# Kernel optimization log

Hardware: AMD Instinct MI355X
Metric: run time of the kernel (lower is better)

The kernel has to match this reference:

```python
import jax, jax.numpy as jnp
import numpy as np
from jax import lax

HEADS = 4
DIM_HEAD = 32
IH = IW = 64
IH_RED = 32  # image_size // reduce_ratio; F.interpolate(size=int) -> square output


def dw_conv(t, w):
    # depthwise 3x3, stride 1, padding 1, NCHW; w: [C,1,3,3]
    return lax.conv_general_dilated(t, w, (1, 1), [(1, 1), (1, 1)],
                                    feature_group_count=t.shape[1],
                                    dimension_numbers=("NCHW", "OIHW", "NCHW"))


def pw_conv(t, w):
    # pointwise 1x1 conv as einsum; w: [O,C,1,1]
    return jnp.einsum("oc,bchw->bohw", w[:, :, 0, 0], t)


def resize_bilinear_ac(t, out_h, out_w):
    # bilinear, align_corners=True, t: [B,C,H,W]
    H, W = t.shape[-2], t.shape[-1]
    ys = jnp.linspace(0.0, H - 1.0, out_h)
    xs = jnp.linspace(0.0, W - 1.0, out_w)
    y0 = jnp.floor(ys).astype(jnp.int32)
    x0 = jnp.floor(xs).astype(jnp.int32)
    y1 = jnp.minimum(y0 + 1, H - 1)
    x1 = jnp.minimum(x0 + 1, W - 1)
    wy = (ys - y0).astype(t.dtype)[None, None, :, None]
    wx = (xs - x0).astype(t.dtype)[None, None, None, :]
    row = t[:, :, y0, :] * (1 - wy) + t[:, :, y1, :] * wy  # [B,C,OH,W]
    out = row[:, :, :, x0] * (1 - wx) + row[:, :, :, x1] * wx  # [B,C,OH,OW]
    return out


def to_heads(t):
    # [B, h*d, H, W] -> [B, h, H*W, d]
    B, _, H, W = t.shape
    return t.reshape(B, HEADS, DIM_HEAD, H * W).transpose(0, 1, 3, 2)


def setup_inputs() -> dict:
    key = jax.random.key(0)
    ks = jax.random.split(key, 7)
    inner = HEADS * DIM_HEAD  # 128
    return {
        "x": jax.random.normal(ks[0], (8, 256, 16, 16), jnp.float32),
        "skip": jax.random.normal(ks[1], (8, 128, 64, 64), jnp.float32),
        "dw_q": jax.random.normal(ks[2], (128, 1, 3, 3), jnp.float32) * 0.1,
        "pw_q": jax.random.normal(ks[3], (inner, 128, 1, 1), jnp.float32) * 0.05,
        "dw_kv": jax.random.normal(ks[4], (256, 1, 3, 3), jnp.float32) * 0.1,
        "pw_kv": jax.random.normal(ks[5], (2 * inner, 256, 1, 1), jnp.float32) * 0.05,
        "w_out": jax.random.normal(ks[6], (128, inner, 1, 1), jnp.float32) * 0.05,
    }


def reference(x, skip, dw_q, pw_q, dw_kv, pw_kv, w_out):
    scale = DIM_HEAD ** -0.5
    q = to_heads(pw_conv(dw_conv(skip, dw_q), pw_q))  # [B,h,4096,d]
    kv = pw_conv(dw_conv(x, dw_kv), pw_kv)            # [B,2*inner,16,16]
    k, v = jnp.split(kv, 2, axis=1)
    k = to_heads(resize_bilinear_ac(k, IH_RED, IH_RED))  # [B,h,1024,d]
    v = to_heads(resize_bilinear_ac(v, IH_RED, IH_RED))
    dots = jnp.einsum("bhqd,bhkd->bhqk", q, k) * scale
    attn = jax.nn.softmax(dots, axis=-1)
    out = jnp.einsum("bhqk,bhkd->bhqd", attn, v)  # [B,h,4096,d]
    B = out.shape[0]
    out = out.transpose(0, 1, 3, 2).reshape(B, HEADS * DIM_HEAD, IH, IW)
    return pw_conv(out, w_out)
```

## Files before the change

kernel.cpp:

```cpp
#include <hip/hip_runtime.h>
#include <hip/hip_bf16.h>

typedef __attribute__((ext_vector_type(4))) float f32x4;
typedef __attribute__((ext_vector_type(8))) short bf16x8;
typedef __attribute__((ext_vector_type(4))) short s16x4;

#define DEV static __device__ __forceinline__

DEV int imin(int a, int b) { return a < b ? a : b; }

DEV short f2bf(float f) {
  union { float f; unsigned u; } v; v.f = f;
  unsigned r = (v.u + 0x7fffu + ((v.u >> 16) & 1u)) >> 16;
  return (short)r;
}

DEV bf16x8 cvt8(const float* __restrict__ p) {
  f32x4 a = *reinterpret_cast<const f32x4*>(p);
  f32x4 b = *reinterpret_cast<const f32x4*>(p + 4);
  bf16x8 r;
  r[0] = f2bf(a[0]); r[1] = f2bf(a[1]); r[2] = f2bf(a[2]); r[3] = f2bf(a[3]);
  r[4] = f2bf(b[0]); r[5] = f2bf(b[1]); r[6] = f2bf(b[2]); r[7] = f2bf(b[3]);
  return r;
}

__global__ __launch_bounds__(256) void k_qgen(const float* __restrict__ skip,
    const float* __restrict__ dw_q, const float* __restrict__ pw_q,
    short* __restrict__ Q) {
  const int b = blockIdx.y;
  const int y = blockIdx.x;
  __shared__ __align__(16) short dwT[64][136];
  const int t = threadIdx.x;
  {
    const int x = t & 63;
    const int cg = t >> 6;
    for (int i = 0; i < 32; ++i) {
      const int c = cg * 32 + i;
      const float* sp = skip + (b * 128 + c) * 4096;
      const float* wp = dw_q + c * 9;
      float acc = 0.f;
      #pragma unroll
      for (int ky = 0; ky < 3; ++ky) {
        const int yy = y + ky - 1;
        if (yy < 0 || yy > 63) continue;
        #pragma unroll
        for (int kx = 0; kx < 3; ++kx) {
          const int xx = x + kx - 1;
          if (xx < 0 || xx > 63) continue;
          acc += sp[yy * 64 + xx] * wp[ky * 3 + kx];
        }
      }
      dwT[x][c] = f2bf(acc);
    }
  }
  __syncthreads();
  const int w = t >> 6, l = t & 63, lr = l & 15, lg = l >> 4;
  f32x4 acc[4][2];
  #pragma unroll
  for (int pt = 0; pt < 4; ++pt)
    #pragma unroll
    for (int ot = 0; ot < 2; ++ot) acc[pt][ot] = f32x4{0.f, 0.f, 0.f, 0.f};
  #pragma unroll
  for (int kk = 0; kk < 4; ++kk) {
    const int c0 = kk * 32 + lg * 8;
    bf16x8 bfr[2];
    #pragma unroll
    for (int ot = 0; ot < 2; ++ot) {
      const int o = (2 * w + ot) * 16 + lr;
      bfr[ot] = cvt8(pw_q + o * 128 + c0);
    }
    #pragma unroll
    for (int pt = 0; pt < 4; ++pt) {
      bf16x8 afr = *reinterpret_cast<const bf16x8*>(&dwT[pt * 16 + lr][c0]);
      #pragma unroll
      for (int ot = 0; ot < 2; ++ot)
        acc[pt][ot] = __builtin_amdgcn_mfma_f32_16x16x32_bf16(afr, bfr[ot], acc[pt][ot], 0, 0, 0);
    }
  }
  const float sc = 0.17677669529663689f;
  #pragma unroll
  for (int pt = 0; pt < 4; ++pt)
    #pragma unroll
    for (int ot = 0; ot < 2; ++ot)
      #pragma unroll
      for (int r = 0; r < 4; ++r) {
        const int pix = y * 64 + pt * 16 + lg * 4 + r;
        const int o = (2 * w + ot) * 16 + lr;
        Q[(b * 4096 + pix) * 128 + o] = f2bf(acc[pt][ot][r] * sc);
      }
}

__global__ __launch_bounds__(256) void k_kvgen(const float* __restrict__ x,
    const float* __restrict__ dw_kv, const float* __restrict__ pw_kv,
    float* __restrict__ kv16) {
  const int b = blockIdx.y;
  const int pq = blockIdx.x;
  __shared__ __align__(16) short dwxT[16][264];
  const int t = threadIdx.x;
  {
    const int pl = t & 15;
    const int cg = t >> 4;
    const int py = pq, px = pl;
    for (int i = 0; i < 16; ++i) {
      const int c = cg * 16 + i;
      const float* sp = x + (b * 256 + c) * 256;
      const float* wp = dw_kv + c * 9;
      float acc = 0.f;
      #pragma unroll
      for (int ky = 0; ky < 3; ++ky) {
        const int yy = py + ky - 1;
        if (yy < 0 || yy > 15) continue;
        #pragma unroll
        for (int kx = 0; kx < 3; ++kx) {
          const int xx = px + kx - 1;
          if (xx < 0 || xx > 15) continue;
          acc += sp[yy * 16 + xx] * wp[ky * 3 + kx];
        }
      }
      dwxT[pl][c] = f2bf(acc);
    }
  }
  __syncthreads();
  const int w = t >> 6, l = t & 63, lr = l & 15, lg = l >> 4;
  f32x4 acc[4];
  #pragma unroll
  for (int ot = 0; ot < 4; ++ot) acc[ot] = f32x4{0.f, 0.f, 0.f, 0.f};
  #pragma unroll
  for (int kk = 0; kk < 8; ++kk) {
    const int c0 = kk * 32 + lg * 8;
    bf16x8 bfr = *reinterpret_cast<const bf16x8*>(&dwxT[lr][c0]);
    #pragma unroll
    for (int ot = 0; ot < 4; ++ot) {
      const int o = (w * 4 + ot) * 16 + lr;
      bf16x8 afr = cvt8(pw_kv + o * 256 + c0);
      acc[ot] = __builtin_amdgcn_mfma_f32_16x16x32_bf16(afr, bfr, acc[ot], 0, 0, 0);
    }
  }
  #pragma unroll
  for (int ot = 0; ot < 4; ++ot)
    #pragma unroll
    for (int r = 0; r < 4; ++r) {
      const int o = (w * 4 + ot) * 16 + lg * 4 + r;
      const int pix = pq * 16 + lr;
      kv16[(b * 256 + o) * 256 + pix] = acc[ot][r];
    }
}

DEV float bilin16(const float* __restrict__ p, int key) {
  const int oy = key >> 5, ox = key & 31;
  const float s = 15.f / 31.f;
  const float syf = oy * s, sxf = ox * s;
  const int y0 = (int)syf, x0 = (int)sxf;
  const int y1 = imin(y0 + 1, 15), x1 = imin(x0 + 1, 15);
  const float wy = syf - (float)y0, wx = sxf - (float)x0;
  const float r0 = p[y0 * 16 + x0] * (1.f - wx) + p[y0 * 16 + x1] * wx;
  const float r1 = p[y1 * 16 + x0] * (1.f - wx) + p[y1 * 16 + x1] * wx;
  return r0 * (1.f - wy) + r1 * wy;
}

__global__ __launch_bounds__(256) void k_resize(const float* __restrict__ kv16,
    short* __restrict__ K, short* __restrict__ Vt) {
  const int idx = blockIdx.x * 256 + threadIdx.x;
  {
    const int d = idx & 31;
    int rest = idx >> 5;
    const int key = rest & 1023; rest >>= 10;
    const int h = rest & 3; const int b = rest >> 2;
    const int ch = h * 32 + d;
    K[idx] = f2bf(bilin16(kv16 + (b * 256 + ch) * 256, key));
  }
  {
    const int key = idx & 1023;
    int rest = idx >> 10;
    const int d = rest & 31; rest >>= 5;
    const int h = rest & 3; const int b = rest >> 2;
    const int ch = 128 + h * 32 + d;
    Vt[idx] = f2bf(bilin16(kv16 + (b * 256 + ch) * 256, key));
  }
}

__global__ __launch_bounds__(256) void k_attn(const short* __restrict__ Q,
    const short* __restrict__ Kk, const short* __restrict__ Vt,
    short* __restrict__ att) {
  const int b = blockIdx.z, h = blockIdx.y;
  const int t = threadIdx.x, w = t >> 6, l = t & 63;
  const int lr = l & 15, lg = l >> 4;
  const int q0 = blockIdx.x * 128 + w * 32;
  __shared__ __align__(16) short P[4][16][72];
  const short* Qb = Q + (b * 4096 + q0) * 128 + h * 32;
  const short* Kb = Kk + (b * 4 + h) * 32768;
  const short* Vb = Vt + (b * 4 + h) * 32768;
  bf16x8 qf[2];
  #pragma unroll
  for (int qt = 0; qt < 2; ++qt)
    qf[qt] = *reinterpret_cast<const bf16x8*>(Qb + (qt * 16 + lr) * 128 + lg * 8);
  f32x4 oacc[2][2];
  float ls[2];
  #pragma unroll
  for (int qt = 0; qt < 2; ++qt) {
    oacc[qt][0] = f32x4{0.f, 0.f, 0.f, 0.f};
    oacc[qt][1] = f32x4{0.f, 0.f, 0.f, 0.f};
    ls[qt] = 0.f;
  }
  for (int kc = 0; kc < 1024; kc += 32) {
    bf16x8 kf[2], vf[2];
    #pragma unroll
    for (int tt = 0; tt < 2; ++tt) {
      kf[tt] = *reinterpret_cast<const bf16x8*>(Kb + (kc + tt * 16 + lr) * 32 + lg * 8);
      vf[tt] = *reinterpret_cast<const bf16x8*>(Vb + (tt * 16 + lr) * 1024 + kc + lg * 8);
    }
    #pragma unroll
    for (int qt = 0; qt < 2; ++qt) {
      const f32x4 z = f32x4{0.f, 0.f, 0.f, 0.f};
      f32x4 s0 = __builtin_amdgcn_mfma_f32_16x16x32_bf16(kf[0], qf[qt], z, 0, 0, 0);
      f32x4 s1 = __builtin_amdgcn_mfma_f32_16x16x32_bf16(kf[1], qf[qt], z, 0, 0, 0);
      float p0[4], p1[4];
      #pragma unroll
      for (int r = 0; r < 4; ++r) { p0[r] = __expf(s0[r]); p1[r] = __expf(s1[r]); }
      ls[qt] += ((p0[0] + p0[1]) + (p0[2] + p0[3])) + ((p1[0] + p1[1]) + (p1[2] + p1[3]));
      s16x4 w0, w1;
      #pragma unroll
      for (int r = 0; r < 4; ++r) { w0[r] = f2bf(p0[r]); w1[r] = f2bf(p1[r]); }
      *reinterpret_cast<s16x4*>(&P[w][lr][lg * 4]) = w0;
      *reinterpret_cast<s16x4*>(&P[w][lr][16 + lg * 4]) = w1;
      asm volatile("s_waitcnt lgkmcnt(0)" ::: "memory");
      __builtin_amdgcn_sched_barrier(0);
      bf16x8 pf = *reinterpret_cast<const bf16x8*>(&P[w][lr][lg * 8]);
      __builtin_amdgcn_sched_barrier(0);
      oacc[qt][0] = __builtin_amdgcn_mfma_f32_16x16x32_bf16(pf, vf[0], oacc[qt][0], 0, 0, 0);
      oacc[qt][1] = __builtin_amdgcn_mfma_f32_16x16x32_bf16(pf, vf[1], oacc[qt][1], 0, 0, 0);
    }
  }
  #pragma unroll
  for (int qt = 0; qt < 2; ++qt) {
    float s = ls[qt];
    s += __shfl_xor(s, 16);
    s += __shfl_xor(s, 32);
    const float inv = 1.f / s;
    #pragma unroll
    for (int r = 0; r < 4; ++r) {
      const float invr = __shfl(inv, lg * 4 + r);
      const int qg = q0 + qt * 16 + lg * 4 + r;
      #pragma unroll
      for (int tt = 0; tt < 2; ++tt)
        att[(b * 4096 + qg) * 128 + h * 32 + tt * 16 + lr] = f2bf(oacc[qt][tt][r] * invr);
    }
  }
}

__global__ __launch_bounds__(256) void k_out(const short* __restrict__ att,
    const float* __restrict__ w_out, float* __restrict__ out) {
  const int b = blockIdx.y;
  const int pix0 = blockIdx.x * 64;
  const int t = threadIdx.x, w = t >> 6, l = t & 63, lr = l & 15, lg = l >> 4;
  f32x4 acc[2][4];
  #pragma unroll
  for (int jt = 0; jt < 2; ++jt)
    #pragma unroll
    for (int pt = 0; pt < 4; ++pt) acc[jt][pt] = f32x4{0.f, 0.f, 0.f, 0.f};
  #pragma unroll
  for (int kk = 0; kk < 4; ++kk) {
    const int c0 = kk * 32 + lg * 8;
    bf16x8 bfr[4];
    #pragma unroll
    for (int pt = 0; pt < 4; ++pt)
      bfr[pt] = *reinterpret_cast<const bf16x8*>(att + (b * 4096 + pix0 + pt * 16 + lr) * 128 + c0);
    #pragma unroll
    for (int jt = 0; jt < 2; ++jt) {
      const int j = (2 * w + jt) * 16 + lr;
      bf16x8 afr = cvt8(w_out + j * 128 + c0);
      #pragma unroll
      for (int pt = 0; pt < 4; ++pt)
        acc[jt][pt] = __builtin_amdgcn_mfma_f32_16x16x32_bf16(afr, bfr[pt], acc[jt][pt], 0, 0, 0);
    }
  }
  #pragma unroll
  for (int jt = 0; jt < 2; ++jt)
    #pragma unroll
    for (int pt = 0; pt < 4; ++pt)
      #pragma unroll
      for (int r = 0; r < 4; ++r) {
        const int j = (2 * w + jt) * 16 + lg * 4 + r;
        const int pix = pix0 + pt * 16 + lr;
        out[(b * 128 + j) * 4096 + pix] = acc[jt][pt][r];
      }
}

extern "C" void kernel_launch(void* const* d_in, const int* in_sizes, int n_in,
                              void* d_out, int out_size, void* d_ws, size_t ws_size,
                              hipStream_t stream) {
  const float* x     = (const float*)d_in[0];
  const float* skip  = (const float*)d_in[1];
  const float* dw_q  = (const float*)d_in[2];
  const float* pw_q  = (const float*)d_in[3];
  const float* dw_kv = (const float*)d_in[4];
  const float* pw_kv = (const float*)d_in[5];
  const float* w_out = (const float*)d_in[6];
  float* out = (float*)d_out;
  (void)in_sizes; (void)n_in; (void)out_size; (void)ws_size;

  char* wsb = (char*)d_ws;
  short* Q    = (short*)(wsb);
  float* kv16 = (float*)(wsb + (size_t)(8u << 20));
  short* K    = (short*)(wsb + (size_t)(10u << 20));
  short* Vt   = (short*)(wsb + (size_t)(12u << 20));
  short* att  = (short*)(wsb + (size_t)(14u << 20));

  k_qgen<<<dim3(64, 8), dim3(256), 0, stream>>>(skip, dw_q, pw_q, Q);
  k_kvgen<<<dim3(16, 8), dim3(256), 0, stream>>>(x, dw_kv, pw_kv, kv16);
  k_resize<<<dim3(4096), dim3(256), 0, stream>>>(kv16, K, Vt);
  k_attn<<<dim3(32, 4, 8), dim3(256), 0, stream>>>(Q, K, Vt, att);
  k_out<<<dim3(64, 8), dim3(256), 0, stream>>>(att, w_out, out);
}
```

Baseline: 227.2 us.

## Fuse Q pointwise projection and output projection into attention kernel

Splits Q generation so a separate kernel only computes the depthwise conv, and moves the Q pointwise projection and the final output projection into the attention kernel. Each block now handles 32 queries for all four heads (one wave per head), keeping Q and the attention output in LDS and removing the att round trip and the k_out launch. The change also folds log2(e) into the Q scale so exp2 can replace exp, uses a packed bf16 convert instruction, and applies an XOR swizzle to the P buffer in LDS. In exchange, blocks cover fewer queries, so K/V are reloaded more often per query, and each block recomputes its Q projection and loads the weights again.

After: 204.4 us. -10.0%, faster.

```diff
diff --git a/kernel.cpp b/kernel.cpp
--- a/kernel.cpp
+++ b/kernel.cpp
@@ -3,7 +3,6 @@
 
 typedef __attribute__((ext_vector_type(4))) float f32x4;
 typedef __attribute__((ext_vector_type(8))) short bf16x8;
-typedef __attribute__((ext_vector_type(4))) short s16x4;
 
 #define DEV static __device__ __forceinline__
 
@@ -13,6 +12,12 @@
   union { float f; unsigned u; } v; v.f = f;
   unsigned r = (v.u + 0x7fffu + ((v.u >> 16) & 1u)) >> 16;
   return (short)r;
+}
+
+DEV unsigned pkbf(float lo, float hi) {
+  unsigned r;
+  asm("v_cvt_pk_bf16_f32 %0, %1, %2" : "=v"(r) : "v"(lo), "v"(hi));
+  return r;
 }
 
 DEV bf16x8 cvt8(const float* __restrict__ p) {
@@ -24,18 +29,24 @@
   return r;
 }
 
-__global__ __launch_bounds__(256) void k_qgen(const float* __restrict__ skip,
-    const float* __restrict__ dw_q, const float* __restrict__ pw_q,
-    short* __restrict__ Q) {
-  const int b = blockIdx.y;
-  const int y = blockIdx.x;
-  __shared__ __align__(16) short dwT[64][136];
+DEV int swz(int q, int c) {
+  return q * 64 + ((((c >> 1) ^ (q & 3)) << 4) | ((c & 1) << 3));
+}
+DEV int swz_rd(int q, int pair) {
+  return q * 64 + ((pair ^ (q & 3)) << 4);
+}
+
+__global__ __launch_bounds__(256) void k_dwq(const float* __restrict__ skip,
+    const float* __restrict__ dw_q, short* __restrict__ dwQ) {
+  const int b = blockIdx.z, cq = blockIdx.y, y = blockIdx.x;
+  __shared__ __align__(16) short T[64][40];
   const int t = threadIdx.x;
   {
-    const int x = t & 63;
-    const int cg = t >> 6;
-    for (int i = 0; i < 32; ++i) {
-      const int c = cg * 32 + i;
+    const int x = t & 63, cg = t >> 6;
+    #pragma unroll
+    for (int i = 0; i < 8; ++i) {
+      const int cl = cg * 8 + i;
+      const int c = cq * 32 + cl;
       const float* sp = skip + (b * 128 + c) * 4096;
       const float* wp = dw_q + c * 9;
       float acc = 0.f;
@@ -50,44 +61,13 @@
           acc += sp[yy * 64 + xx] * wp[ky * 3 + kx];
         }
       }
-      dwT[x][c] = f2bf(acc);
+      T[x][cl] = f2bf(acc);
     }
   }
   __syncthreads();
-  const int w = t >> 6, l = t & 63, lr = l & 15, lg = l >> 4;
-  f32x4 acc[4][2];
-  #pragma unroll
-  for (int pt = 0; pt < 4; ++pt)
-    #pragma unroll
-    for (int ot = 0; ot < 2; ++ot) acc[pt][ot] = f32x4{0.f, 0.f, 0.f, 0.f};
-  #pragma unroll
-  for (int kk = 0; kk < 4; ++kk) {
-    const int c0 = kk * 32 + lg * 8;
-    bf16x8 bfr[2];
-    #pragma unroll
-    for (int ot = 0; ot < 2; ++ot) {
-      const int o = (2 * w + ot) * 16 + lr;
-      bfr[ot] = cvt8(pw_q + o * 128 + c0);
-    }
-    #pragma unroll
-    for (int pt = 0; pt < 4; ++pt) {
-      bf16x8 afr = *reinterpret_cast<const bf16x8*>(&dwT[pt * 16 + lr][c0]);
-      #pragma unroll
-      for (int ot = 0; ot < 2; ++ot)
-        acc[pt][ot] = __builtin_amdgcn_mfma_f32_16x16x32_bf16(afr, bfr[ot], acc[pt][ot], 0, 0, 0);
-    }
-  }
-  const float sc = 0.17677669529663689f;
-  #pragma unroll
-  for (int pt = 0; pt < 4; ++pt)
-    #pragma unroll
-    for (int ot = 0; ot < 2; ++ot)
-      #pragma unroll
-      for (int r = 0; r < 4; ++r) {
-        const int pix = y * 64 + pt * 16 + lg * 4 + r;
-        const int o = (2 * w + ot) * 16 + lr;
-        Q[(b * 4096 + pix) * 128 + o] = f2bf(acc[pt][ot][r] * sc);
-      }
+  const int x2 = t >> 2, cc = t & 3;
+  bf16x8 v = *reinterpret_cast<const bf16x8*>(&T[x2][cc * 8]);
+  *reinterpret_cast<bf16x8*>(dwQ + (b * 4096 + y * 64 + x2) * 128 + cq * 32 + cc * 8) = v;
 }
 
 __global__ __launch_bounds__(256) void k_kvgen(const float* __restrict__ x,
@@ -179,21 +159,75 @@
   }
 }
 
-__global__ __launch_bounds__(256) void k_attn(const short* __restrict__ Q,
-    const short* __restrict__ Kk, const short* __restrict__ Vt,
-    short* __restrict__ att) {
-  const int b = blockIdx.z, h = blockIdx.y;
-  const int t = threadIdx.x, w = t >> 6, l = t & 63;
+__global__ __launch_bounds__(256) void k_attn(const short* __restrict__ dwQ,
+    const float* __restrict__ pw_q, const short* __restrict__ Kk,
+    const short* __restrict__ Vt, const float* __restrict__ w_out,
+    float* __restrict__ out) {
+  const int b = blockIdx.y;
+  const int q0 = blockIdx.x * 32;
+  const int t = threadIdx.x, h = t >> 6, l = t & 63;
   const int lr = l & 15, lg = l >> 4;
-  const int q0 = blockIdx.x * 128 + w * 32;
-  __shared__ __align__(16) short P[4][16][72];
-  const short* Qb = Q + (b * 4096 + q0) * 128 + h * 32;
+  __shared__ __align__(16) short QT[32][136];
+  __shared__ __align__(16) char QS[4][2048];
+  __shared__ __align__(16) char PS[4][1024];
+  __shared__ __align__(16) short AT[32][136];
+
+  {
+    const int rr = t >> 4, c16 = t & 15;
+    #pragma unroll
+    for (int i = 0; i < 2; ++i) {
+      const int q = rr + i * 16;
+      bf16x8 v = *reinterpret_cast<const bf16x8*>(dwQ + (b * 4096 + q0 + q) * 128 + c16 * 8);
+      *reinterpret_cast<bf16x8*>(&QT[q][c16 * 8]) = v;
+    }
+  }
+  __syncthreads();
+
+  {
+    f32x4 aq[2][2];
+    #pragma unroll
+    for (int ot = 0; ot < 2; ++ot)
+      #pragma unroll
+      for (int qt = 0; qt < 2; ++qt) aq[ot][qt] = f32x4{0.f, 0.f, 0.f, 0.f};
+    #pragma unroll
+    for (int kk = 0; kk < 4; ++kk) {
+      const int c0 = kk * 32 + lg * 8;
+      bf16x8 bfr[2];
+      #pragma unroll
+      for (int qt = 0; qt < 2; ++qt)
+        bfr[qt] = *reinterpret_cast<const bf16x8*>(&QT[qt * 16 + lr][c0]);
+      #pragma unroll
+      for (int ot = 0; ot < 2; ++ot) {
+        bf16x8 afr = cvt8(pw_q + ((h * 2 + ot) * 16 + lr) * 128 + c0);
+        #pragma unroll
+        for (int qt = 0; qt < 2; ++qt)
+          aq[ot][qt] = __builtin_amdgcn_mfma_f32_16x16x32_bf16(afr, bfr[qt], aq[ot][qt], 0, 0, 0);
+      }
+    }
+    const float qs = 0.25505403f;
+    #pragma unroll
+    for (int ot = 0; ot < 2; ++ot)
+      #pragma unroll
+      for (int qt = 0; qt < 2; ++qt) {
+        unsigned d0 = pkbf(aq[ot][qt][0] * qs, aq[ot][qt][1] * qs);
+        unsigned d1 = pkbf(aq[ot][qt][2] * qs, aq[ot][qt][3] * qs);
+        const int q = qt * 16 + lr, c = ot * 4 + lg;
+        *reinterpret_cast<unsigned long long*>(QS[h] + swz(q, c)) =
+            ((unsigned long long)d1 << 32) | d0;
+      }
+  }
+  asm volatile("s_waitcnt lgkmcnt(0)" ::: "memory");
+  __builtin_amdgcn_sched_barrier(0);
+  bf16x8 qf[2];
+  #pragma unroll
+  for (int qt = 0; qt < 2; ++qt) {
+    const int q = qt * 16 + lr;
+    qf[qt] = *reinterpret_cast<const bf16x8*>(QS[h] + swz_rd(q, lg));
+  }
+  __builtin_amdgcn_sched_barrier(0);
+
   const short* Kb = Kk + (b * 4 + h) * 32768;
   const short* Vb = Vt + (b * 4 + h) * 32768;
-  bf16x8 qf[2];
-  #pragma unroll
-  for (int qt = 0; qt < 2; ++qt)
-    qf[qt] = *reinterpret_cast<const bf16x8*>(Qb + (qt * 16 + lr) * 128 + lg * 8);
   f32x4 oacc[2][2];
   float ls[2];
   #pragma unroll
@@ -216,21 +250,26 @@
       f32x4 s1 = __builtin_amdgcn_mfma_f32_16x16x32_bf16(kf[1], qf[qt], z, 0, 0, 0);
       float p0[4], p1[4];
       #pragma unroll
-      for (int r = 0; r < 4; ++r) { p0[r] = __expf(s0[r]); p1[r] = __expf(s1[r]); }
+      for (int r = 0; r < 4; ++r) {
+        p0[r] = __builtin_amdgcn_exp2f(s0[r]);
+        p1[r] = __builtin_amdgcn_exp2f(s1[r]);
+      }
       ls[qt] += ((p0[0] + p0[1]) + (p0[2] + p0[3])) + ((p1[0] + p1[1]) + (p1[2] + p1[3]));
-      s16x4 w0, w1;
-      #pragma unroll
-      for (int r = 0; r < 4; ++r) { w0[r] = f2bf(p0[r]); w1[r] = f2bf(p1[r]); }
-      *reinterpret_cast<s16x4*>(&P[w][lr][lg * 4]) = w0;
-      *reinterpret_cast<s16x4*>(&P[w][lr][16 + lg * 4]) = w1;
+      unsigned a0 = pkbf(p0[0], p0[1]), a1 = pkbf(p0[2], p0[3]);
+      unsigned b0 = pkbf(p1[0], p1[1]), b1 = pkbf(p1[2], p1[3]);
+      *reinterpret_cast<unsigned long long*>(PS[h] + swz(lr, lg)) =
+          ((unsigned long long)a1 << 32) | a0;
+      *reinterpret_cast<unsigned long long*>(PS[h] + swz(lr, lg + 4)) =
+          ((unsigned long long)b1 << 32) | b0;
       asm volatile("s_waitcnt lgkmcnt(0)" ::: "memory");
       __builtin_amdgcn_sched_barrier(0);
-      bf16x8 pf = *reinterpret_cast<const bf16x8*>(&P[w][lr][lg * 8]);
+      bf16x8 pf = *reinterpret_cast<const bf16x8*>(PS[h] + swz_rd(lr, lg));
       __builtin_amdgcn_sched_barrier(0);
       oacc[qt][0] = __builtin_amdgcn_mfma_f32_16x16x32_bf16(pf, vf[0], oacc[qt][0], 0, 0, 0);
       oacc[qt][1] = __builtin_amdgcn_mfma_f32_16x16x32_bf16(pf, vf[1], oacc[qt][1], 0, 0, 0);
     }
   }
+
   #pragma unroll
   for (int qt = 0; qt < 2; ++qt) {
     float s = ls[qt];
@@ -240,49 +279,42 @@
     #pragma unroll
     for (int r = 0; r < 4; ++r) {
       const float invr = __shfl(inv, lg * 4 + r);
-      const int qg = q0 + qt * 16 + lg * 4 + r;
+      const int q = qt * 16 + lg * 4 + r;
       #pragma unroll
       for (int tt = 0; tt < 2; ++tt)
-        att[(b * 4096 + qg) * 128 + h * 32 + tt * 16 + lr] = f2bf(oacc[qt][tt][r] * invr);
-    }
-  }
-}
-
-__global__ __launch_bounds__(256) void k_out(const short* __restrict__ att,
-    const float* __restrict__ w_out, float* __restrict__ out) {
-  const int b = blockIdx.y;
-  const int pix0 = blockIdx.x * 64;
-  const int t = threadIdx.x, w = t >> 6, l = t & 63, lr = l & 15, lg = l >> 4;
-  f32x4 acc[2][4];
+        AT[q][h * 32 + tt * 16 + lr] = f2bf(oacc[qt][tt][r] * invr);
+    }
+  }
+  __syncthreads();
+
+  f32x4 ao[2][2];
   #pragma unroll
   for (int jt = 0; jt < 2; ++jt)
     #pragma unroll
-    for (int pt = 0; pt < 4; ++pt) acc[jt][pt] = f32x4{0.f, 0.f, 0.f, 0.f};
+    for (int qt = 0; qt < 2; ++qt) ao[jt][qt] = f32x4{0.f, 0.f, 0.f, 0.f};
   #pragma unroll
   for (int kk = 0; kk < 4; ++kk) {
     const int c0 = kk * 32 + lg * 8;
-    bf16x8 bfr[4];
-    #pragma unroll
-    for (int pt = 0; pt < 4; ++pt)
-      bfr[pt] = *reinterpret_cast<const bf16x8*>(att + (b * 4096 + pix0 + pt * 16 + lr) * 128 + c0);
+    bf16x8 bfr[2];
+    #pragma unroll
+    for (int qt = 0; qt < 2; ++qt)
+      bfr[qt] = *reinterpret_cast<const bf16x8*>(&AT[qt * 16 + lr][c0]);
     #pragma unroll
     for (int jt = 0; jt < 2; ++jt) {
-      const int j = (2 * w + jt) * 16 + lr;
-      bf16x8 afr = cvt8(w_out + j * 128 + c0);
-      #pragma unroll
-      for (int pt = 0; pt < 4; ++pt)
-        acc[jt][pt] = __builtin_amdgcn_mfma_f32_16x16x32_bf16(afr, bfr[pt], acc[jt][pt], 0, 0, 0);
+      bf16x8 afr = cvt8(w_out + ((h * 2 + jt) * 16 + lr) * 128 + c0);
+      #pragma unroll
+      for (int qt = 0; qt < 2; ++qt)
+        ao[jt][qt] = __builtin_amdgcn_mfma_f32_16x16x32_bf16(afr, bfr[qt], ao[jt][qt], 0, 0, 0);
     }
   }
   #pragma unroll
   for (int jt = 0; jt < 2; ++jt)
     #pragma unroll
-    for (int pt = 0; pt < 4; ++pt)
+    for (int qt = 0; qt < 2; ++qt)
       #pragma unroll
       for (int r = 0; r < 4; ++r) {
-        const int j = (2 * w + jt) * 16 + lg * 4 + r;
-        const int pix = pix0 + pt * 16 + lr;
-        out[(b * 128 + j) * 4096 + pix] = acc[jt][pt][r];
+        const int j = (h * 2 + jt) * 16 + lg * 4 + r;
+        out[(b * 128 + j) * 4096 + q0 + qt * 16 + lr] = ao[jt][qt][r];
       }
 }
 
@@ -300,15 +332,13 @@
   (void)in_sizes; (void)n_in; (void)out_size; (void)ws_size;
 
   char* wsb = (char*)d_ws;
-  short* Q    = (short*)(wsb);
+  short* dwQ  = (short*)(wsb);
   float* kv16 = (float*)(wsb + (size_t)(8u << 20));
   short* K    = (short*)(wsb + (size_t)(10u << 20));
   short* Vt   = (short*)(wsb + (size_t)(12u << 20));
-  short* att  = (short*)(wsb + (size_t)(14u << 20));
-
-  k_qgen<<<dim3(64, 8), dim3(256), 0, stream>>>(skip, dw_q, pw_q, Q);
+
+  k_dwq<<<dim3(64, 4, 8), dim3(256), 0, stream>>>(skip, dw_q, dwQ);
   k_kvgen<<<dim3(16, 8), dim3(256), 0, stream>>>(x, dw_kv, pw_kv, kv16);
   k_resize<<<dim3(4096), dim3(256), 0, stream>>>(kv16, K, Vt);
-  k_attn<<<dim3(32, 4, 8), dim3(256), 0, stream>>>(Q, K, Vt, att);
-  k_out<<<dim3(64, 8), dim3(256), 0, stream>>>(att, w_out, out);
-}
+  k_attn<<<dim3(128, 8), dim3(256), 0, stream>>>(dwQ, pw_q, K, Vt, w_out, out);
+}
```
